# Kernel tuning notes

Measured on AMD Instinct MI355X. Metric: run time of the kernel, lower is better.

Reference implementation:

```python
import jax, jax.numpy as jnp
import numpy as np

EPS = 1e-12  # torch F.normalize eps

def _l2norm(t):
    # normalize over last axis (tokens N), matching F.normalize(dim=-1)
    n = jnp.sqrt(jnp.sum(t * t, axis=-1, keepdims=True))
    return t / jnp.maximum(n, EPS)

def setup_inputs() -> dict:
    key = jax.random.key(0)
    ks = jax.random.split(key, 4)
    B, N, C, H = 16, 3136, 768, 16
    x = jax.random.normal(ks[0], (B, N, C), dtype=jnp.float32)
    w_qkv = jax.random.normal(ks[1], (3 * C, C), dtype=jnp.float32) * (C ** -0.5)
    temperature = jnp.ones((H, 1, 1), dtype=jnp.float32)
    w_proj = jax.random.normal(ks[2], (C, C), dtype=jnp.float32) * (C ** -0.5)
    b_proj = jnp.zeros((C,), dtype=jnp.float32)
    return {"x": x, "w_qkv": w_qkv, "temperature": temperature,
            "w_proj": w_proj, "b_proj": b_proj}

def reference(x, w_qkv, temperature, w_proj, b_proj):
    B, N, C = x.shape
    H = temperature.shape[0]
    dh = C // H
    # qkv: [B,N,3C] -> [B,N,3,H,dh] -> [3,B,H,dh,N]
    qkv = (x @ w_qkv.T).reshape(B, N, 3, H, dh)
    qkv = jnp.transpose(qkv, (2, 0, 3, 4, 1))
    q, k, v = qkv[0], qkv[1], qkv[2]          # each [B,H,dh,N]
    q = _l2norm(q)
    k = _l2norm(k)
    # cross-covariance attention over channel axis: [B,H,dh,dh]
    attn = jnp.einsum('bhdn,bhen->bhde', q, k) * temperature
    attn = jax.nn.softmax(attn, axis=-1)
    out = jnp.einsum('bhde,bhen->bhdn', attn, v)  # [B,H,dh,N]
    out = jnp.transpose(out, (0, 3, 1, 2)).reshape(B, N, C)
    return out @ w_proj.T + b_proj
```

## Files before the change

kernel.cpp:

```cpp
#include <hip/hip_runtime.h>
#include <hip/hip_bf16.h>
#include <stdint.h>

using f32x4   = __attribute__((ext_vector_type(4))) float;
using half8   = __attribute__((ext_vector_type(8))) _Float16;
using half4   = __attribute__((ext_vector_type(4))) _Float16;
using float4v = __attribute__((ext_vector_type(4))) float;

typedef const __attribute__((address_space(1))) void gas_void;
typedef __attribute__((address_space(3))) void las_void;

__device__ __forceinline__ void gload_lds16(const void* gptr, void* lptr) {
  __builtin_amdgcn_global_load_lds((gas_void*)(uintptr_t)gptr,
                                   (las_void*)(uintptr_t)lptr, 16, 0, 0);
}

#define MFMA_F16(a, b, c) __builtin_amdgcn_mfma_f32_16x16x32_f16((a), (b), (c), 0, 0, 0)

__global__ void k_cvtw(const float* __restrict__ wqkv, const float* __restrict__ wproj,
                       _Float16* __restrict__ w16, _Float16* __restrict__ wp16,
                       _Float16* __restrict__ wvT) {
  const long N1 = 221184L, N2 = 73728L, N3 = 98304L;
  const long total = N1 + N2 + N3;
  for (long i = (long)blockIdx.x * blockDim.x + threadIdx.x; i < total;
       i += (long)gridDim.x * blockDim.x) {
    if (i < N1 + N2) {
      const float* src; _Float16* dst; long off;
      if (i < N1) { src = wqkv;  dst = w16;  off = i; }
      else        { src = wproj; dst = wp16; off = i - N1; }
      const float4v* p = (const float4v*)(src + off * 8);
      float4v a = p[0], b = p[1];
      half8 o;
      o[0] = (_Float16)a[0]; o[1] = (_Float16)a[1]; o[2] = (_Float16)a[2]; o[3] = (_Float16)a[3];
      o[4] = (_Float16)b[0]; o[5] = (_Float16)b[1]; o[6] = (_Float16)b[2]; o[7] = (_Float16)b[3];
      *(half8*)(dst + off * 8) = o;
    } else {
      const long u = i - N1 - N2;
      const int h = (int)(u / 6144);
      const int r = (int)(u % 6144);
      const int f = r >> 3, e0 = (r & 7) * 8;
      half8 o;
      if (e0 >= 48) {
#pragma unroll
        for (int j = 0; j < 8; ++j) o[j] = (_Float16)0.f;
      } else {
#pragma unroll
        for (int j = 0; j < 8; ++j)
          o[j] = (_Float16)wqkv[(long)(1536 + h * 48 + e0 + j) * 768 + f];
      }
      *(half8*)(wvT + ((long)(h * 768 + f) * 64 + e0)) = o;
    }
  }
}

__global__ __launch_bounds__(256)
void k_cvtx(const float* __restrict__ x, _Float16* __restrict__ x16,
            _Float16* __restrict__ xT) {
  __shared__ _Float16 lt[64 * 68];
  const int bid = blockIdx.x;
  const int b = bid / 588;
  const int rem = bid % 588;
  const int tt = rem / 12, ct = rem % 12;
  const long t0g = (long)b * 3136 + tt * 64;
  const int c0 = ct * 64;
  const int tid = threadIdx.x;
#pragma unroll
  for (int ch = 0; ch < 4; ++ch) {
    const int idx = tid + ch * 256;
    const int tr = idx >> 4, cg = (idx & 15) * 4;
    float4v v = *(const float4v*)&x[(t0g + tr) * 768 + c0 + cg];
    half4 hv;
    hv[0] = (_Float16)v[0]; hv[1] = (_Float16)v[1];
    hv[2] = (_Float16)v[2]; hv[3] = (_Float16)v[3];
    *(half4*)&x16[(t0g + tr) * 768 + c0 + cg] = hv;
    *(half4*)&lt[tr * 68 + cg] = hv;
  }
  __syncthreads();
  const int c = tid >> 2, tch = tid & 3;
  half8 o0, o1;
#pragma unroll
  for (int j = 0; j < 8; ++j) o0[j] = lt[(tch * 16 + j) * 68 + c];
#pragma unroll
  for (int j = 0; j < 8; ++j) o1[j] = lt[(tch * 16 + 8 + j) * 68 + c];
  _Float16* dst = xT + (long)b * 2408448 + (long)(c0 + c) * 3136 + tt * 64 + tch * 16;
  *(half8*)dst = o0;
  *(half8*)(dst + 8) = o1;
}

__global__ __launch_bounds__(256)
void k_gram(const _Float16* __restrict__ xT, _Float16* __restrict__ G) {
  __shared__ _Float16 lds[2][2][128 * 32];
  const int tid = threadIdx.x;
  const int wv = tid >> 6, lane = tid & 63;
  const int g = lane >> 4, cidx = lane & 15;
  const int wr = wv >> 1, wc = wv & 1;

  const int nwg = (int)gridDim.x;
  const int q = nwg >> 3, r = nwg & 7;
  const int xcd = (int)blockIdx.x & 7, bidx = (int)blockIdx.x >> 3;
  int wg = (xcd < r ? xcd * (q + 1) : r * (q + 1) + (xcd - r) * q) + bidx;
  const int b = wg / 21;
  int p = wg % 21;
  int mt = 0;
  while (p >= 6 - mt) { p -= 6 - mt; ++mt; }
  const int nt = mt + p;

  const _Float16* Ab = xT + (long)b * 2408448 + (long)mt * 128 * 3136;
  const _Float16* Bb = xT + (long)b * 2408448 + (long)nt * 128 * 3136;

  const int srow = lane >> 2;
  const int sgr  = (lane & 3) ^ ((lane >> 3) & 3);

  auto stage = [&](int buf, int kt) {
#pragma unroll
    for (int l = 0; l < 2; ++l) {
      const int rbase = wv * 32 + l * 16;
      const long koff = (long)kt * 32 + sgr * 8;
      gload_lds16(Ab + (long)(rbase + srow) * 3136 + koff, &lds[buf][0][rbase * 32]);
      gload_lds16(Bb + (long)(rbase + srow) * 3136 + koff, &lds[buf][1][rbase * 32]);
    }
  };
  const int gr = (g ^ ((cidx >> 1) & 3)) * 8;

  f32x4 acc[4][4] = {};
  stage(0, 0);
  __syncthreads();
  for (int kt = 0; kt < 98; ++kt) {
    const int cur = kt & 1;
    if (kt + 1 < 98) stage(cur ^ 1, kt + 1);
    half8 af[4], bf[4];
#pragma unroll
    for (int m = 0; m < 4; ++m)
      af[m] = *(const half8*)&lds[cur][0][(wr * 64 + m * 16 + cidx) * 32 + gr];
#pragma unroll
    for (int n = 0; n < 4; ++n)
      bf[n] = *(const half8*)&lds[cur][1][(wc * 64 + n * 16 + cidx) * 32 + gr];
#pragma unroll
    for (int m = 0; m < 4; ++m)
#pragma unroll
      for (int n = 0; n < 4; ++n)
        acc[m][n] = MFMA_F16(af[m], bf[n], acc[m][n]);
    __syncthreads();
  }
  _Float16* Gb = G + (long)b * 589824;
  const long m0 = (long)mt * 128, n0 = (long)nt * 128;
#pragma unroll
  for (int m = 0; m < 4; ++m)
#pragma unroll
    for (int rr = 0; rr < 4; ++rr) {
      const long row = m0 + wr * 64 + m * 16 + g * 4 + rr;
#pragma unroll
      for (int n = 0; n < 4; ++n)
        Gb[row * 768 + n0 + wc * 64 + n * 16 + cidx] = (_Float16)acc[m][n][rr];
    }
  if (mt != nt) {
#pragma unroll
    for (int m = 0; m < 4; ++m)
#pragma unroll
      for (int n = 0; n < 4; ++n) {
        half4 hv;
#pragma unroll
        for (int rr = 0; rr < 4; ++rr) hv[rr] = (_Float16)acc[m][n][rr];
        const long col  = n0 + wc * 64 + n * 16 + cidx;
        const long row0 = m0 + wr * 64 + m * 16 + g * 4;
        *(half4*)&Gb[col * 768 + row0] = hv;
      }
  }
}

template<bool OUT_F32>
__global__ __launch_bounds__(256)
void k_g128(const _Float16* __restrict__ A, const _Float16* __restrict__ B,
            void* __restrict__ Cv, const float* __restrict__ bias,
            int Mt, int Nt, long Areal, long Astr, long Bstr, long Cstr,
            long N, long K)
{
  __shared__ _Float16 lds[2][2][128 * 32];
  const int tid = threadIdx.x;
  const int wv = tid >> 6, lane = tid & 63;
  const int g = lane >> 4, cidx = lane & 15;
  const int wr = wv >> 1, wc = wv & 1;

  const int nwg = (int)gridDim.x;
  const int q = nwg >> 3, r = nwg & 7;
  const int xcd = (int)blockIdx.x & 7, bidx = (int)blockIdx.x >> 3;
  int wg = (xcd < r ? xcd * (q + 1) : r * (q + 1) + (xcd - r) * q) + bidx;
  const int tpb = Mt * Nt;
  const int b = wg / tpb;
  const int rem = wg % tpb;
  const int mt = rem % Mt, nt = rem / Mt;
  const long m0 = (long)mt * 128, n0 = (long)nt * 128;

  const _Float16* Ab = A + b * Astr + m0 * K;
  const _Float16* Bb = B + b * Bstr + n0 * K;
  const int nkt = (int)(K >> 5);

  const int srow = lane >> 2;
  const int sgr  = (lane & 3) ^ ((lane >> 3) & 3);

  auto stage = [&](int buf, int kt) {
#pragma unroll
    for (int l = 0; l < 2; ++l) {
      const int rbase = wv * 32 + l * 16;
      const long koff = (long)kt * 32 + sgr * 8;
      gload_lds16(Ab + (long)(rbase + srow) * K + koff, &lds[buf][0][rbase * 32]);
      gload_lds16(Bb + (long)(rbase + srow) * K + koff, &lds[buf][1][rbase * 32]);
    }
  };
  const int gr = (g ^ ((cidx >> 1) & 3)) * 8;

  f32x4 acc[4][4] = {};
  stage(0, 0);
  __syncthreads();
  for (int kt = 0; kt < nkt; ++kt) {
    const int cur = kt & 1;
    if (kt + 1 < nkt) stage(cur ^ 1, kt + 1);
    half8 af[4], bf[4];
#pragma unroll
    for (int m = 0; m < 4; ++m)
      af[m] = *(const half8*)&lds[cur][0][(wr * 64 + m * 16 + cidx) * 32 + gr];
#pragma unroll
    for (int n = 0; n < 4; ++n)
      bf[n] = *(const half8*)&lds[cur][1][(wc * 64 + n * 16 + cidx) * 32 + gr];
#pragma unroll
    for (int m = 0; m < 4; ++m)
#pragma unroll
      for (int n = 0; n < 4; ++n)
        acc[m][n] = MFMA_F16(af[m], bf[n], acc[m][n]);
    __syncthreads();
  }

  float bv[4] = {0.f, 0.f, 0.f, 0.f};
  if (bias) {
#pragma unroll
    for (int n = 0; n < 4; ++n) bv[n] = bias[n0 + wc * 64 + n * 16 + cidx];
  }
  if constexpr (OUT_F32) {
    float* C = (float*)Cv + b * Cstr;
#pragma unroll
    for (int m = 0; m < 4; ++m)
#pragma unroll
      for (int rr = 0; rr < 4; ++rr) {
        const long row = m0 + wr * 64 + m * 16 + g * 4 + rr;
        if (row < Areal) {
#pragma unroll
          for (int n = 0; n < 4; ++n)
            C[row * N + n0 + wc * 64 + n * 16 + cidx] = acc[m][n][rr] + bv[n];
        }
      }
  } else {
    _Float16* C = (_Float16*)Cv + b * Cstr;
#pragma unroll
    for (int m = 0; m < 4; ++m)
#pragma unroll
      for (int rr = 0; rr < 4; ++rr) {
        const long row = m0 + wr * 64 + m * 16 + g * 4 + rr;
        if (row < Areal) {
#pragma unroll
          for (int n = 0; n < 4; ++n)
            C[row * N + n0 + wc * 64 + n * 16 + cidx] = (_Float16)acc[m][n][rr];
        }
      }
  }
}

__global__ __launch_bounds__(256)
void k_heads(const _Float16* __restrict__ QG, const _Float16* __restrict__ w16,
             const _Float16* __restrict__ wvT, const float* __restrict__ temperature,
             _Float16* __restrict__ weffT)
{
  const int b = blockIdx.x >> 4, h = blockIdx.x & 15;
  const int tid = threadIdx.x;
  const int w = tid >> 6, lane = tid & 63;
  const int g = lane >> 4, c = lane & 15;

  __shared__ float red[4][48 * 48];
  __shared__ float redss[4][2][48];
  __shared__ float inv[2][48];
  __shared__ _Float16 Pb[48 * 64];

  const _Float16* QGq = QG + (long)b * 1179648 + (long)(h * 48) * 768;
  const _Float16* QGk = QGq + 768L * 768;
  const _Float16* Wq  = w16 + (long)(h * 48) * 768;
  const _Float16* Wk  = w16 + (long)(768 + h * 48) * 768;

  f32x4 aS[3][3] = {};
  f32x4 aq[3] = {};
  f32x4 ak[3] = {};
  for (int ks = w * 6; ks < w * 6 + 6; ++ks) {
    const int k0 = ks * 32 + g * 8;
    half8 t1[3], t3[3], wqf[3], wkf[3];
#pragma unroll
    for (int m = 0; m < 3; ++m) {
      const long ro = (long)(m * 16 + c) * 768 + k0;
      t1[m]  = *(const half8*)(QGq + ro);
      t3[m]  = *(const half8*)(QGk + ro);
      wqf[m] = *(const half8*)(Wq + ro);
      wkf[m] = *(const half8*)(Wk + ro);
    }
#pragma unroll
    for (int m = 0; m < 3; ++m) {
      aq[m] = MFMA_F16(t1[m], wqf[m], aq[m]);
      ak[m] = MFMA_F16(t3[m], wkf[m], ak[m]);
#pragma unroll
      for (int n = 0; n < 3; ++n)
        aS[m][n] = MFMA_F16(t1[m], wkf[n], aS[m][n]);
    }
  }

#pragma unroll
  for (int m = 0; m < 3; ++m) {
#pragma unroll
    for (int n = 0; n < 3; ++n)
#pragma unroll
      for (int rr = 0; rr < 4; ++rr)
        red[w][(m * 16 + g * 4 + rr) * 48 + n * 16 + c] = aS[m][n][rr];
#pragma unroll
    for (int rr = 0; rr < 4; ++rr)
      if (c == g * 4 + rr) {
        redss[w][0][m * 16 + c] = aq[m][rr];
        redss[w][1][m * 16 + c] = ak[m][rr];
      }
  }
  __syncthreads();

  if (tid < 96) {
    const int is_k = tid / 48, d = tid % 48;
    const float s = redss[0][is_k][d] + redss[1][is_k][d] + redss[2][is_k][d] + redss[3][is_k][d];
    inv[is_k][d] = 1.0f / fmaxf(sqrtf(s), 1e-12f);
  }
  __syncthreads();

  if (tid < 48) {
    const int d = tid;
    const float iq = inv[0][d] * temperature[h];
    float rowv[48];
    float mx = -3.0e38f;
#pragma unroll
    for (int e = 0; e < 48; ++e) {
      const int idx = d * 48 + e;
      float t = (red[0][idx] + red[1][idx] + red[2][idx] + red[3][idx]) * iq * inv[1][e];
      rowv[e] = t;
      mx = fmaxf(mx, t);
    }
    float sum = 0.f;
#pragma unroll
    for (int e = 0; e < 48; ++e) {
      const float pv = __expf(rowv[e] - mx);
      rowv[e] = pv;
      sum += pv;
    }
    const float is = 1.0f / sum;
#pragma unroll
    for (int e = 0; e < 48; ++e)
      Pb[d * 64 + e] = (_Float16)(rowv[e] * is);
#pragma unroll
    for (int e = 48; e < 64; ++e)
      Pb[d * 64 + e] = (_Float16)0.f;
  }
  __syncthreads();

  half8 pf[3][2];
#pragma unroll
  for (int nf = 0; nf < 3; ++nf)
#pragma unroll
    for (int ks = 0; ks < 2; ++ks)
      pf[nf][ks] = *(const half8*)&Pb[(nf * 16 + c) * 64 + ks * 32 + g * 8];

  const _Float16* wvh = wvT + (long)h * 768 * 64;
  _Float16* wout = weffT + (long)b * 589824 + h * 48;

  for (int m = 0; m < 12; ++m) {
    const int f0 = w * 192 + m * 16;
    half8 va[2];
#pragma unroll
    for (int ks = 0; ks < 2; ++ks)
      va[ks] = *(const half8*)&wvh[(long)(f0 + c) * 64 + ks * 32 + g * 8];
    f32x4 a3[3] = {};
#pragma unroll
    for (int ks = 0; ks < 2; ++ks)
#pragma unroll
      for (int nf = 0; nf < 3; ++nf)
        a3[nf] = MFMA_F16(va[ks], pf[nf][ks], a3[nf]);
#pragma unroll
    for (int nf = 0; nf < 3; ++nf)
#pragma unroll
      for (int rr = 0; rr < 4; ++rr)
        wout[(long)(f0 + g * 4 + rr) * 768 + nf * 16 + c] = (_Float16)a3[nf][rr];
  }
}

extern "C" void kernel_launch(void* const* d_in, const int* in_sizes, int n_in,
                              void* d_out, int out_size, void* d_ws, size_t ws_size,
                              hipStream_t stream)
{
  (void)in_sizes; (void)n_in; (void)out_size; (void)ws_size;
  const float* x      = (const float*)d_in[0];
  const float* w_qkv  = (const float*)d_in[1];
  const float* temp   = (const float*)d_in[2];
  const float* w_proj = (const float*)d_in[3];
  const float* b_proj = (const float*)d_in[4];
  float* out = (float*)d_out;

  char* ws = (char*)d_ws;
  _Float16* x16   = (_Float16*)(ws);
  _Float16* xT    = (_Float16*)(ws + 77070336L);
  _Float16* G     = (_Float16*)(ws + 154140672L);
  _Float16* QG    = (_Float16*)(ws + 173015040L);
  _Float16* weffT = (_Float16*)(ws + 210763776L);
  _Float16* wfin  = (_Float16*)(ws + 229638144L);
  _Float16* w16   = (_Float16*)(ws + 248512512L);
  _Float16* wp16  = (_Float16*)(ws + 252051456L);
  _Float16* wvT   = (_Float16*)(ws + 253231104L);

  k_cvtw<<<768, 256, 0, stream>>>(w_qkv, w_proj, w16, wp16, wvT);
  k_cvtx<<<9408, 256, 0, stream>>>(x, x16, xT);
  k_gram<<<336, 256, 0, stream>>>(xT, G);
  k_g128<false><<<1152, 256, 0, stream>>>(w16, G, QG, nullptr,
                                          12, 6, 1536, 0, 589824, 1179648, 768, 768);
  k_heads<<<256, 256, 0, stream>>>(QG, w16, wvT, temp, weffT);
  k_g128<false><<<576, 256, 0, stream>>>(wp16, weffT, wfin, nullptr,
                                         6, 6, 768, 0, 589824, 589824, 768, 768);
  k_g128<true><<<2400, 256, 0, stream>>>(x16, wfin, out, b_proj,
                                         25, 6, 3136, 3136L * 768, 589824, 3136L * 768,
                                         768, 768);
}
```

Measured before the change: 339.9 us.

## Fuse per-head QG GEMM into heads kernel and use 256-tile final GEMM

Removes the separate QG = W·G batched GEMM kernel and instead computes each head's 48x768 slice of W·G inside the heads kernel, staged in LDS with an XOR swizzle, then forms the q/k Gram products and norms from it. The final output GEMM moves to a new 256x256-tile kernel with 512 threads and XCD-aware block remapping. This is meant to cut the QG round trip through global memory and launch overhead, and to raise data reuse in the largest GEMM. In exchange each heads block now redoes a 48x768x768 GEMM per pass and uses a large LDS footprint, which limits occupancy on a 256-block grid.

After: 409.1 us. 20.4% more time.

```diff
diff --git a/kernel.cpp b/kernel.cpp
--- a/kernel.cpp
+++ b/kernel.cpp
@@ -264,65 +264,213 @@
   }
 }
 
-__global__ __launch_bounds__(256)
-void k_heads(const _Float16* __restrict__ QG, const _Float16* __restrict__ w16,
-             const _Float16* __restrict__ wvT, const float* __restrict__ temperature,
-             _Float16* __restrict__ weffT)
+template<bool OUT_F32>
+__global__ __launch_bounds__(512, 2)
+void k_g256(const _Float16* __restrict__ A, const _Float16* __restrict__ B,
+            void* __restrict__ Cv, const float* __restrict__ bias,
+            int Mt, int Nt, long Areal, long Astr, long Bstr, long Cstr,
+            long N, long K)
+{
+  __shared__ _Float16 lds[2][2][256 * 32];
+  const int tid = threadIdx.x;
+  const int wv = tid >> 6, lane = tid & 63;
+  const int g = lane >> 4, cidx = lane & 15;
+  const int wr = wv >> 2, wc = wv & 3;
+
+  const int nwg = (int)gridDim.x;
+  const int q = nwg >> 3, r = nwg & 7;
+  const int xcd = (int)blockIdx.x & 7, bidx = (int)blockIdx.x >> 3;
+  int wg = (xcd < r ? xcd * (q + 1) : r * (q + 1) + (xcd - r) * q) + bidx;
+  const int tpb = Mt * Nt;
+  const int b = wg / tpb;
+  const int rem = wg % tpb;
+  const int mt = rem % Mt, nt = rem / Mt;
+  const long m0 = (long)mt * 256, n0 = (long)nt * 256;
+
+  const _Float16* Ab = A + b * Astr + m0 * K;
+  const _Float16* Bb = B + b * Bstr + n0 * K;
+  const int nkt = (int)(K >> 5);
+
+  const int srow = lane >> 2;
+  const int sgr  = (lane & 3) ^ ((lane >> 3) & 3);
+
+  auto stage = [&](int buf, int kt) {
+    const long koff = (long)kt * 32 + sgr * 8;
+#pragma unroll
+    for (int l = 0; l < 2; ++l) {
+      const int chunk = l * 8 + wv;
+      const long ro = (long)(chunk * 16 + srow);
+      gload_lds16(Ab + ro * K + koff, &lds[buf][0][chunk * 512]);
+      gload_lds16(Bb + ro * K + koff, &lds[buf][1][chunk * 512]);
+    }
+  };
+  const int gr = (g ^ ((cidx >> 1) & 3)) * 8;
+
+  f32x4 acc[8][4] = {};
+  stage(0, 0);
+  __syncthreads();
+  for (int kt = 0; kt < nkt; ++kt) {
+    const int cur = kt & 1;
+    if (kt + 1 < nkt) stage(cur ^ 1, kt + 1);
+    half8 af[8], bf[4];
+#pragma unroll
+    for (int m = 0; m < 8; ++m)
+      af[m] = *(const half8*)&lds[cur][0][(wr * 128 + m * 16 + cidx) * 32 + gr];
+#pragma unroll
+    for (int n = 0; n < 4; ++n)
+      bf[n] = *(const half8*)&lds[cur][1][(wc * 64 + n * 16 + cidx) * 32 + gr];
+#pragma unroll
+    for (int m = 0; m < 8; ++m)
+#pragma unroll
+      for (int n = 0; n < 4; ++n)
+        acc[m][n] = MFMA_F16(af[m], bf[n], acc[m][n]);
+    __syncthreads();
+  }
+
+  float bv[4] = {0.f, 0.f, 0.f, 0.f};
+  if (bias) {
+#pragma unroll
+    for (int n = 0; n < 4; ++n) bv[n] = bias[n0 + wc * 64 + n * 16 + cidx];
+  }
+  if constexpr (OUT_F32) {
+    float* C = (float*)Cv + b * Cstr;
+#pragma unroll
+    for (int m = 0; m < 8; ++m)
+#pragma unroll
+      for (int rr = 0; rr < 4; ++rr) {
+        const long row = m0 + wr * 128 + m * 16 + g * 4 + rr;
+        if (row < Areal) {
+#pragma unroll
+          for (int n = 0; n < 4; ++n)
+            C[row * N + n0 + wc * 64 + n * 16 + cidx] = acc[m][n][rr] + bv[n];
+        }
+      }
+  } else {
+    _Float16* C = (_Float16*)Cv + b * Cstr;
+#pragma unroll
+    for (int m = 0; m < 8; ++m)
+#pragma unroll
+      for (int rr = 0; rr < 4; ++rr) {
+        const long row = m0 + wr * 128 + m * 16 + g * 4 + rr;
+        if (row < Areal) {
+#pragma unroll
+          for (int n = 0; n < 4; ++n)
+            C[row * N + n0 + wc * 64 + n * 16 + cidx] = (_Float16)acc[m][n][rr];
+        }
+      }
+  }
+}
+
+__global__ __launch_bounds__(512)
+void k_heads2(const _Float16* __restrict__ G, const _Float16* __restrict__ w16,
+              const _Float16* __restrict__ wvT, const float* __restrict__ temperature,
+              _Float16* __restrict__ weffT)
 {
   const int b = blockIdx.x >> 4, h = blockIdx.x & 15;
   const int tid = threadIdx.x;
   const int w = tid >> 6, lane = tid & 63;
   const int g = lane >> 4, c = lane & 15;
 
+  __shared__ _Float16 T1s[48 * 768];
   __shared__ float red[4][48 * 48];
   __shared__ float redss[4][2][48];
   __shared__ float inv[2][48];
   __shared__ _Float16 Pb[48 * 64];
 
-  const _Float16* QGq = QG + (long)b * 1179648 + (long)(h * 48) * 768;
-  const _Float16* QGk = QGq + 768L * 768;
-  const _Float16* Wq  = w16 + (long)(h * 48) * 768;
-  const _Float16* Wk  = w16 + (long)(768 + h * 48) * 768;
-
-  f32x4 aS[3][3] = {};
-  f32x4 aq[3] = {};
-  f32x4 ak[3] = {};
-  for (int ks = w * 6; ks < w * 6 + 6; ++ks) {
-    const int k0 = ks * 32 + g * 8;
-    half8 t1[3], t3[3], wqf[3], wkf[3];
-#pragma unroll
-    for (int m = 0; m < 3; ++m) {
-      const long ro = (long)(m * 16 + c) * 768 + k0;
-      t1[m]  = *(const half8*)(QGq + ro);
-      t3[m]  = *(const half8*)(QGk + ro);
-      wqf[m] = *(const half8*)(Wq + ro);
-      wkf[m] = *(const half8*)(Wk + ro);
-    }
-#pragma unroll
-    for (int m = 0; m < 3; ++m) {
-      aq[m] = MFMA_F16(t1[m], wqf[m], aq[m]);
-      ak[m] = MFMA_F16(t3[m], wkf[m], ak[m]);
-#pragma unroll
-      for (int n = 0; n < 3; ++n)
-        aS[m][n] = MFMA_F16(t1[m], wkf[n], aS[m][n]);
-    }
-  }
-
-#pragma unroll
-  for (int m = 0; m < 3; ++m) {
-#pragma unroll
-    for (int n = 0; n < 3; ++n)
-#pragma unroll
-      for (int rr = 0; rr < 4; ++rr)
-        red[w][(m * 16 + g * 4 + rr) * 48 + n * 16 + c] = aS[m][n][rr];
-#pragma unroll
-    for (int rr = 0; rr < 4; ++rr)
-      if (c == g * 4 + rr) {
-        redss[w][0][m * 16 + c] = aq[m][rr];
-        redss[w][1][m * 16 + c] = ak[m][rr];
-      }
-  }
-  __syncthreads();
+  const _Float16* Gb = G + (long)b * 589824;
+  const _Float16* Wq = w16 + (long)(h * 48) * 768;
+  const _Float16* Wk = w16 + (long)(768 + h * 48) * 768;
+
+  for (int pass = 0; pass < 2; ++pass) {
+    const _Float16* Wa = pass ? Wk : Wq;
+    f32x4 accT[3][6] = {};
+#pragma unroll 2
+    for (int ks = 0; ks < 24; ++ks) {
+      const int k0 = ks * 32 + g * 8;
+      half8 a[3], bfr[6];
+#pragma unroll
+      for (int m = 0; m < 3; ++m)
+        a[m] = *(const half8*)&Wa[(long)(m * 16 + c) * 768 + k0];
+#pragma unroll
+      for (int n = 0; n < 6; ++n)
+        bfr[n] = *(const half8*)&Gb[(long)(w * 96 + n * 16 + c) * 768 + k0];
+#pragma unroll
+      for (int m = 0; m < 3; ++m)
+#pragma unroll
+        for (int n = 0; n < 6; ++n)
+          accT[m][n] = MFMA_F16(a[m], bfr[n], accT[m][n]);
+    }
+#pragma unroll
+    for (int m = 0; m < 3; ++m)
+#pragma unroll
+      for (int n = 0; n < 6; ++n)
+#pragma unroll
+        for (int rr = 0; rr < 4; ++rr) {
+          const int d = m * 16 + g * 4 + rr;
+          const int col = w * 96 + n * 16 + c;
+          const int u = d * 96 + ((col >> 3) ^ (d & 7));
+          T1s[u * 8 + (col & 7)] = (_Float16)accT[m][n][rr];
+        }
+    __syncthreads();
+    if (w < 4) {
+      if (pass == 0) {
+        f32x4 aS[3][3] = {};
+        f32x4 aq[3] = {};
+        for (int ks = w * 6; ks < w * 6 + 6; ++ks) {
+          const int k0 = ks * 32 + g * 8;
+          const int cg = ks * 4 + g;
+          half8 at[3], bk[3], bq[3];
+#pragma unroll
+          for (int m = 0; m < 3; ++m) {
+            const int d = m * 16 + c;
+            at[m] = *(const half8*)&T1s[(d * 96 + (cg ^ (d & 7))) * 8];
+            bk[m] = *(const half8*)&Wk[(long)(m * 16 + c) * 768 + k0];
+            bq[m] = *(const half8*)&Wq[(long)(m * 16 + c) * 768 + k0];
+          }
+#pragma unroll
+          for (int m = 0; m < 3; ++m) {
+            aq[m] = MFMA_F16(at[m], bq[m], aq[m]);
+#pragma unroll
+            for (int n = 0; n < 3; ++n)
+              aS[m][n] = MFMA_F16(at[m], bk[n], aS[m][n]);
+          }
+        }
+#pragma unroll
+        for (int m = 0; m < 3; ++m) {
+#pragma unroll
+          for (int n = 0; n < 3; ++n)
+#pragma unroll
+            for (int rr = 0; rr < 4; ++rr)
+              red[w][(m * 16 + g * 4 + rr) * 48 + n * 16 + c] = aS[m][n][rr];
+#pragma unroll
+          for (int rr = 0; rr < 4; ++rr)
+            if (c == g * 4 + rr) redss[w][0][m * 16 + c] = aq[m][rr];
+        }
+      } else {
+        f32x4 ak[3] = {};
+        for (int ks = w * 6; ks < w * 6 + 6; ++ks) {
+          const int k0 = ks * 32 + g * 8;
+          const int cg = ks * 4 + g;
+          half8 at[3], bk[3];
+#pragma unroll
+          for (int m = 0; m < 3; ++m) {
+            const int d = m * 16 + c;
+            at[m] = *(const half8*)&T1s[(d * 96 + (cg ^ (d & 7))) * 8];
+            bk[m] = *(const half8*)&Wk[(long)(m * 16 + c) * 768 + k0];
+          }
+#pragma unroll
+          for (int m = 0; m < 3; ++m)
+            ak[m] = MFMA_F16(at[m], bk[m], ak[m]);
+        }
+#pragma unroll
+        for (int m = 0; m < 3; ++m)
+#pragma unroll
+          for (int rr = 0; rr < 4; ++rr)
+            if (c == g * 4 + rr) redss[w][1][m * 16 + c] = ak[m][rr];
+      }
+    }
+    __syncthreads();
+  }
 
   if (tid < 96) {
     const int is_k = tid / 48, d = tid % 48;
@@ -330,7 +478,6 @@
     inv[is_k][d] = 1.0f / fmaxf(sqrtf(s), 1e-12f);
   }
   __syncthreads();
-
   if (tid < 48) {
     const int d = tid;
     const float iq = inv[0][d] * temperature[h];
@@ -370,8 +517,8 @@
   const _Float16* wvh = wvT + (long)h * 768 * 64;
   _Float16* wout = weffT + (long)b * 589824 + h * 48;
 
-  for (int m = 0; m < 12; ++m) {
-    const int f0 = w * 192 + m * 16;
+  for (int mi = 0; mi < 6; ++mi) {
+    const int f0 = w * 96 + mi * 16;
     half8 va[2];
 #pragma unroll
     for (int ks = 0; ks < 2; ++ks)
@@ -406,7 +553,6 @@
   _Float16* x16   = (_Float16*)(ws);
   _Float16* xT    = (_Float16*)(ws + 77070336L);
   _Float16* G     = (_Float16*)(ws + 154140672L);
-  _Float16* QG    = (_Float16*)(ws + 173015040L);
   _Float16* weffT = (_Float16*)(ws + 210763776L);
   _Float16* wfin  = (_Float16*)(ws + 229638144L);
   _Float16* w16   = (_Float16*)(ws + 248512512L);
@@ -416,12 +562,10 @@
   k_cvtw<<<768, 256, 0, stream>>>(w_qkv, w_proj, w16, wp16, wvT);
   k_cvtx<<<9408, 256, 0, stream>>>(x, x16, xT);
   k_gram<<<336, 256, 0, stream>>>(xT, G);
-  k_g128<false><<<1152, 256, 0, stream>>>(w16, G, QG, nullptr,
-                                          12, 6, 1536, 0, 589824, 1179648, 768, 768);
-  k_heads<<<256, 256, 0, stream>>>(QG, w16, wvT, temp, weffT);
+  k_heads2<<<256, 512, 0, stream>>>(G, w16, wvT, temp, weffT);
   k_g128<false><<<576, 256, 0, stream>>>(wp16, weffT, wfin, nullptr,
                                          6, 6, 768, 0, 589824, 589824, 768, 768);
-  k_g128<true><<<2400, 256, 0, stream>>>(x16, wfin, out, b_proj,
-                                         25, 6, 3136, 3136L * 768, 589824, 3136L * 768,
-                                         768, 768);
-}
+  k_g256<true><<<624, 512, 0, stream>>>(x16, wfin, out, b_proj,
+                                        13, 3, 3136, 3136L * 768, 589824, 3136L * 768,
+                                        768, 768);
+}
```
